# Kernel optimization log

Measured on AMD Instinct MI355X. Metric: run time of the kernel, lower is better.

## Reference

```python
import jax, jax.numpy as jnp
import numpy as np

BATCH = 4096
IN_SIZES = [1024, 1024, 1024, 1024]
EMB = 2048  # embracement_size


def setup_inputs() -> dict:
    key = jax.random.key(0)
    keys = jax.random.split(key, 3 * len(IN_SIZES))
    inp = {}
    for i, d in enumerate(IN_SIZES):
        inp[f"x{i}"] = jax.random.normal(keys[3 * i], (BATCH, d), dtype=jnp.float32)
        # Linear params (Kaiming-ish scale)
        inp[f"W{i}"] = jax.random.normal(keys[3 * i + 1], (d, EMB), dtype=jnp.float32) / np.sqrt(d)
        inp[f"b{i}"] = jax.random.normal(keys[3 * i + 2], (EMB,), dtype=jnp.float32) * 0.01
    return inp


def _sample_indices(batch, num_feats, emb):
    # availabilities=None, selection_probabilities=None -> uniform p over modalities
    # multinomial(p, num_samples=emb, replacement=True) == categorical over log p
    logits = jnp.zeros((batch, num_feats), dtype=jnp.float32)  # uniform
    k = jax.random.key(42)
    # shape (emb, batch) broadcasts against logits batch shape (batch,)
    idx = jax.random.categorical(k, logits, axis=-1, shape=(emb, batch))
    return idx.T  # [batch, emb]


def reference(x0, W0, b0, x1, W1, b1, x2, W2, b2, x3, W3, b3):
    xs = [x0, x1, x2, x3]
    Ws = [W0, W1, W2, W3]
    bs = [b0, b1, b2, b3]
    # docking: Linear + ReLU per modality -> [batch, EMB, num_feats]
    dock = jnp.stack([jax.nn.relu(x @ W + b) for x, W, b in zip(xs, Ws, bs)], axis=-1)
    B, E, F = dock.shape
    idx = _sample_indices(B, F, E)  # [B, E] int32
    # gather along modality axis (replaces one-hot multiply-sum)
    out = jnp.take_along_axis(dock, idx[:, :, None], axis=-1)[..., 0]
    return out  # [batch, EMB]
```

## Files before the change

### kernel.cpp

```cpp
#include <hip/hip_runtime.h>
#include <stdint.h>


typedef short short8 __attribute__((ext_vector_type(8)));
typedef float floatx4 __attribute__((ext_vector_type(4)));

#define B_DIM 4096
#define K_DIM 1024
#define E_DIM 2048

__device__ __forceinline__ uint16_t f2bf(float x) {
  uint32_t u = __float_as_uint(x);
  u += 0x7FFFu + ((u >> 16) & 1u);
  return (uint16_t)(u >> 16);
}

__device__ __forceinline__ void threefry(uint32_t x0, uint32_t x1,
                                         uint32_t& o0, uint32_t& o1) {
  const uint32_t ks0 = 0u;
  const uint32_t ks1 = 42u;
  const uint32_t ks2 = 0x1BD11BDAu ^ 42u;
  x0 += ks0; x1 += ks1;
#define TF_R(r) { x0 += x1; x1 = (x1 << r) | (x1 >> (32 - r)); x1 ^= x0; }
  TF_R(13) TF_R(15) TF_R(26) TF_R(6)
  x0 += ks1; x1 += ks2 + 1u;
  TF_R(17) TF_R(29) TF_R(16) TF_R(24)
  x0 += ks2; x1 += ks0 + 2u;
  TF_R(13) TF_R(15) TF_R(26) TF_R(6)
  x0 += ks0; x1 += ks1 + 3u;
  TF_R(17) TF_R(29) TF_R(16) TF_R(24)
  x0 += ks1; x1 += ks2 + 4u;
  TF_R(13) TF_R(15) TF_R(26) TF_R(6)
  x0 += ks2; x1 += ks0 + 5u;
#undef TF_R
  o0 = x0; o1 = x1;
}

__global__ __launch_bounds__(256) void prep_kernel(
    const float* __restrict__ x0, const float* __restrict__ x1,
    const float* __restrict__ x2, const float* __restrict__ x3,
    const float* __restrict__ W0, const float* __restrict__ W1,
    const float* __restrict__ W2, const float* __restrict__ W3,
    uint16_t* __restrict__ xb, uint16_t* __restrict__ Wt,
    uint32_t* __restrict__ idx2) {
  __shared__ float tile[32][33];
  const uint32_t g = blockIdx.x;
  const uint32_t chunk = g / 13u, slot = g % 13u;
  const int t = threadIdx.x;

  if (slot == 0) {
    uint32_t tid = chunk * 256u + t;
    uint32_t base = tid << 6;
    uint32_t word = 0;
#pragma unroll 4
    for (int j = 0; j < 16; ++j) {
      uint32_t c = base + 4u * j;
      uint32_t best = 0, bi = 0;
#pragma unroll
      for (uint32_t f = 0; f < 4; ++f) {
        uint32_t y0, y1;
        threefry(0u, c + f, y0, y1);
        uint32_t m = (y0 ^ y1) >> 9;
        if (f == 0) best = m;
        else if (m > best) { best = m; bi = f; }
      }
      word |= bi << (2 * j);
    }
    idx2[tid] = word;
  } else if (slot <= 8) {
    uint32_t xi = chunk * 8u + (slot - 1);
    int f = xi >> 12;
    const float* x = (f == 0) ? x0 : (f == 1) ? x1 : (f == 2) ? x2 : x3;
    size_t i = ((size_t)(xi & 4095) * 256 + t) * 4;
    float4 v = *(const float4*)(x + i);
    union { uint16_t h[4]; uint64_t q; } p;
    p.h[0] = f2bf(v.x); p.h[1] = f2bf(v.y);
    p.h[2] = f2bf(v.z); p.h[3] = f2bf(v.w);
    *(uint64_t*)(xb + (size_t)f * B_DIM * K_DIM + i) = p.q;
  } else {
    uint32_t wi = chunk * 4u + (slot - 9);
    int f = wi >> 11;
    uint32_t ip = wi & 2047;
    const float* W = (f == 0) ? W0 : (f == 1) ? W1 : (f == 2) ? W2 : W3;
    int e0 = (ip & 63) * 32, k0 = (ip >> 6) * 32;
    int tx = t & 31, ty = t >> 5;
#pragma unroll
    for (int i = 0; i < 4; ++i)
      tile[ty + i * 8][tx] = W[(size_t)(k0 + ty + i * 8) * E_DIM + e0 + tx];
    __syncthreads();
    int el = t >> 3, kc = (t & 7) * 4;
    union { uint16_t h[4]; uint64_t q; } p;
#pragma unroll
    for (int i = 0; i < 4; ++i) p.h[i] = f2bf(tile[kc + i][el]);
    uint16_t* dst = Wt + (size_t)f * E_DIM * K_DIM;
    *(uint64_t*)(dst + (size_t)(e0 + el) * K_DIM + k0 + kc) = p.q;
  }
}

__device__ __forceinline__ void async16(const uint16_t* g, uint16_t* lds) {
  __builtin_amdgcn_global_load_lds(
      (const __attribute__((address_space(1))) void*)g,
      (__attribute__((address_space(3))) void*)lds, 16, 0, 0);
}

__global__ __launch_bounds__(512, 4) void gemm_fused(
    const uint16_t* __restrict__ Ab, const uint16_t* __restrict__ Bbt,
    const uint32_t* __restrict__ idx2,
    const float* __restrict__ bias0, const float* __restrict__ bias1,
    const float* __restrict__ bias2, const float* __restrict__ bias3,
    float* __restrict__ out) {
  __shared__ uint16_t As[2][128 * 32];
  __shared__ uint16_t Bs[2][128 * 32];

  const int tid = threadIdx.x;
  const int w = tid >> 6;
  const int l = tid & 63;
  const int mBase = blockIdx.y * 128;
  const int nBase = blockIdx.x * 128;

  const int wm = (w >> 2) * 64;
  const int wn = (w & 3) * 32;
  const int sr = l >> 2;
  const int sc8 = (l & 3) ^ ((l >> 3) & 3);
  const int fr = l & 15, fq = l >> 4;
  const int fqs = (fq ^ ((fr >> 1) & 3)) * 8;

  const int b_hi0 = (mBase + wm) >> 4;
  uint32_t iw[2][4];
#pragma unroll
  for (int ni = 0; ni < 2; ++ni) {
    int col = nBase + wn + ni * 16 + fr;
#pragma unroll
    for (int mi = 0; mi < 4; ++mi)
      iw[ni][mi] = idx2[(size_t)col * (B_DIM / 16) + b_hi0 + mi];
  }

  floatx4 res[4][2] = {};

#pragma unroll 1
  for (int f = 0; f < 4; ++f) {
    const uint16_t* A = Ab  + (size_t)f * B_DIM * K_DIM + (size_t)mBase * K_DIM;
    const uint16_t* B = Bbt + (size_t)f * E_DIM * K_DIM + (size_t)nBase * K_DIM;
    const uint16_t* Aw = A + (size_t)(16 * w + sr) * K_DIM + sc8 * 8;
    const uint16_t* Bw = B + (size_t)(16 * w + sr) * K_DIM + sc8 * 8;

    floatx4 acc[4][2] = {};

    async16(Aw, &As[0][w * 512]);
    async16(Bw, &Bs[0][w * 512]);
    __syncthreads();

    int buf = 0;
#pragma unroll 1
    for (int kt = 0; kt < 32; ++kt) {
      int k0 = kt * 32;
      if (kt + 1 < 32) {
        async16(Aw + k0 + 32, &As[buf ^ 1][w * 512]);
        async16(Bw + k0 + 32, &Bs[buf ^ 1][w * 512]);
      }
      short8 a[4], b[2];
      #pragma unroll
      for (int mi = 0; mi < 4; ++mi)
        a[mi] = *(const short8*)&As[buf][(wm + mi * 16 + fr) * 32 + fqs];
      #pragma unroll
      for (int ni = 0; ni < 2; ++ni)
        b[ni] = *(const short8*)&Bs[buf][(wn + ni * 16 + fr) * 32 + fqs];
      #pragma unroll
      for (int mi = 0; mi < 4; ++mi)
        #pragma unroll
        for (int ni = 0; ni < 2; ++ni)
          acc[mi][ni] = __builtin_amdgcn_mfma_f32_16x16x32_bf16(
              a[mi], b[ni], acc[mi][ni], 0, 0, 0);
      __syncthreads();
      buf ^= 1;
    }

    const float* bias = (f == 0) ? bias0 : (f == 1) ? bias1
                      : (f == 2) ? bias2 : bias3;
    #pragma unroll
    for (int ni = 0; ni < 2; ++ni) {
      float bvf = bias[nBase + wn + ni * 16 + fr];
      #pragma unroll
      for (int mi = 0; mi < 4; ++mi) {
        uint32_t wd = iw[ni][mi];
        #pragma unroll
        for (int r = 0; r < 4; ++r) {
          uint32_t sel = (wd >> (2 * (fq * 4 + r))) & 3u;
          if (sel == (uint32_t)f) res[mi][ni][r] = acc[mi][ni][r] + bvf;
        }
      }
    }
  }

#pragma unroll
  for (int ni = 0; ni < 2; ++ni) {
    int col = nBase + wn + ni * 16 + fr;
#pragma unroll
    for (int mi = 0; mi < 4; ++mi) {
      int row0 = mBase + wm + mi * 16 + fq * 4;
#pragma unroll
      for (int r = 0; r < 4; ++r) {
        float o = res[mi][ni][r];
        __builtin_nontemporal_store(o > 0.f ? o : 0.f,
                                    &out[(size_t)(row0 + r) * E_DIM + col]);
      }
    }
  }
}

extern "C" void kernel_launch(void* const* d_in, const int* in_sizes, int n_in,
                              void* d_out, int out_size, void* d_ws, size_t ws_size,
                              hipStream_t stream) {
  const float* x[4]; const float* W[4]; const float* bs[4];
  for (int f = 0; f < 4; ++f) {
    x[f]  = (const float*)d_in[3 * f + 0];
    W[f]  = (const float*)d_in[3 * f + 1];
    bs[f] = (const float*)d_in[3 * f + 2];
  }
  char* ws = (char*)d_ws;
  uint16_t* xb  = (uint16_t*)ws;
  uint16_t* Wt  = (uint16_t*)(ws + (size_t)32 * 1024 * 1024);
  uint32_t* idx2 = (uint32_t*)(ws + (size_t)48 * 1024 * 1024);
  float* out = (float*)d_out;

  prep_kernel<<<dim3(26624), dim3(256), 0, stream>>>(
      x[0], x[1], x[2], x[3], W[0], W[1], W[2], W[3], xb, Wt, idx2);
  gemm_fused<<<dim3(E_DIM / 128, B_DIM / 128), dim3(512), 0, stream>>>(
      xb, Wt, idx2, bs[0], bs[1], bs[2], bs[3], out);
}
```

Before: 303.2 us.

## Use 4 waves with 64x64 warp tiles, drop LDS swizzle, use rotate builtin

```diff
diff --git a/kernel.cpp b/kernel.cpp
--- a/kernel.cpp
+++ b/kernel.cpp
@@ -8,6 +8,12 @@
 #define B_DIM 4096
 #define K_DIM 1024
 #define E_DIM 2048
+
+#if __has_builtin(__builtin_rotateleft32)
+#define ROTL32(x, r) __builtin_rotateleft32((x), (r))
+#else
+#define ROTL32(x, r) __builtin_amdgcn_alignbit((x), (x), 32 - (r))
+#endif
 
 __device__ __forceinline__ uint16_t f2bf(float x) {
   uint32_t u = __float_as_uint(x);
@@ -21,7 +27,7 @@
   const uint32_t ks1 = 42u;
   const uint32_t ks2 = 0x1BD11BDAu ^ 42u;
   x0 += ks0; x1 += ks1;
-#define TF_R(r) { x0 += x1; x1 = (x1 << r) | (x1 >> (32 - r)); x1 ^= x0; }
+#define TF_R(r) { x0 += x1; x1 = ROTL32(x1, r); x1 ^= x0; }
   TF_R(13) TF_R(15) TF_R(26) TF_R(6)
   x0 += ks1; x1 += ks2 + 1u;
   TF_R(17) TF_R(29) TF_R(16) TF_R(24)
@@ -103,7 +109,7 @@
       (__attribute__((address_space(3))) void*)lds, 16, 0, 0);
 }
 
-__global__ __launch_bounds__(512, 4) void gemm_fused(
+__global__ __launch_bounds__(256, 2) void gemm_fused(
     const uint16_t* __restrict__ Ab, const uint16_t* __restrict__ Bbt,
     const uint32_t* __restrict__ idx2,
     const float* __restrict__ bias0, const float* __restrict__ bias1,
@@ -118,57 +124,61 @@
   const int mBase = blockIdx.y * 128;
   const int nBase = blockIdx.x * 128;
 
-  const int wm = (w >> 2) * 64;
-  const int wn = (w & 3) * 32;
-  const int sr = l >> 2;
-  const int sc8 = (l & 3) ^ ((l >> 3) & 3);
+  const int wm = (w >> 1) * 64, wn = (w & 1) * 64;
+  const int sr = l >> 2, sc8 = l & 3;
   const int fr = l & 15, fq = l >> 4;
-  const int fqs = (fq ^ ((fr >> 1) & 3)) * 8;
+  const int c0 = 2 * w, c1 = 2 * w + 1;
 
   const int b_hi0 = (mBase + wm) >> 4;
-  uint32_t iw[2][4];
-#pragma unroll
-  for (int ni = 0; ni < 2; ++ni) {
+  uint32_t iw[4][4];
+#pragma unroll
+  for (int ni = 0; ni < 4; ++ni) {
     int col = nBase + wn + ni * 16 + fr;
 #pragma unroll
     for (int mi = 0; mi < 4; ++mi)
       iw[ni][mi] = idx2[(size_t)col * (B_DIM / 16) + b_hi0 + mi];
   }
 
-  floatx4 res[4][2] = {};
+  floatx4 res[4][4] = {};
 
 #pragma unroll 1
   for (int f = 0; f < 4; ++f) {
     const uint16_t* A = Ab  + (size_t)f * B_DIM * K_DIM + (size_t)mBase * K_DIM;
     const uint16_t* B = Bbt + (size_t)f * E_DIM * K_DIM + (size_t)nBase * K_DIM;
-    const uint16_t* Aw = A + (size_t)(16 * w + sr) * K_DIM + sc8 * 8;
-    const uint16_t* Bw = B + (size_t)(16 * w + sr) * K_DIM + sc8 * 8;
-
-    floatx4 acc[4][2] = {};
-
-    async16(Aw, &As[0][w * 512]);
-    async16(Bw, &Bs[0][w * 512]);
+    const uint16_t* Ap0 = A + (size_t)(c0 * 16 + sr) * K_DIM + sc8 * 8;
+    const uint16_t* Ap1 = A + (size_t)(c1 * 16 + sr) * K_DIM + sc8 * 8;
+    const uint16_t* Bp0 = B + (size_t)(c0 * 16 + sr) * K_DIM + sc8 * 8;
+    const uint16_t* Bp1 = B + (size_t)(c1 * 16 + sr) * K_DIM + sc8 * 8;
+
+    floatx4 acc[4][4] = {};
+
+    async16(Ap0, &As[0][c0 * 512]);
+    async16(Ap1, &As[0][c1 * 512]);
+    async16(Bp0, &Bs[0][c0 * 512]);
+    async16(Bp1, &Bs[0][c1 * 512]);
     __syncthreads();
 
     int buf = 0;
 #pragma unroll 1
     for (int kt = 0; kt < 32; ++kt) {
-      int k0 = kt * 32;
+      int kn = (kt + 1) * 32;
       if (kt + 1 < 32) {
-        async16(Aw + k0 + 32, &As[buf ^ 1][w * 512]);
-        async16(Bw + k0 + 32, &Bs[buf ^ 1][w * 512]);
-      }
-      short8 a[4], b[2];
+        async16(Ap0 + kn, &As[buf ^ 1][c0 * 512]);
+        async16(Ap1 + kn, &As[buf ^ 1][c1 * 512]);
+        async16(Bp0 + kn, &Bs[buf ^ 1][c0 * 512]);
+        async16(Bp1 + kn, &Bs[buf ^ 1][c1 * 512]);
+      }
+      short8 a[4], b[4];
       #pragma unroll
       for (int mi = 0; mi < 4; ++mi)
-        a[mi] = *(const short8*)&As[buf][(wm + mi * 16 + fr) * 32 + fqs];
-      #pragma unroll
-      for (int ni = 0; ni < 2; ++ni)
-        b[ni] = *(const short8*)&Bs[buf][(wn + ni * 16 + fr) * 32 + fqs];
+        a[mi] = *(const short8*)&As[buf][(wm + mi * 16 + fr) * 32 + fq * 8];
+      #pragma unroll
+      for (int ni = 0; ni < 4; ++ni)
+        b[ni] = *(const short8*)&Bs[buf][(wn + ni * 16 + fr) * 32 + fq * 8];
       #pragma unroll
       for (int mi = 0; mi < 4; ++mi)
         #pragma unroll
-        for (int ni = 0; ni < 2; ++ni)
+        for (int ni = 0; ni < 4; ++ni)
           acc[mi][ni] = __builtin_amdgcn_mfma_f32_16x16x32_bf16(
               a[mi], b[ni], acc[mi][ni], 0, 0, 0);
       __syncthreads();
@@ -178,7 +188,7 @@
     const float* bias = (f == 0) ? bias0 : (f == 1) ? bias1
                       : (f == 2) ? bias2 : bias3;
     #pragma unroll
-    for (int ni = 0; ni < 2; ++ni) {
+    for (int ni = 0; ni < 4; ++ni) {
       float bvf = bias[nBase + wn + ni * 16 + fr];
       #pragma unroll
       for (int mi = 0; mi < 4; ++mi) {
@@ -193,7 +203,7 @@
   }
 
 #pragma unroll
-  for (int ni = 0; ni < 2; ++ni) {
+  for (int ni = 0; ni < 4; ++ni) {
     int col = nBase + wn + ni * 16 + fr;
 #pragma unroll
     for (int mi = 0; mi < 4; ++mi) {
@@ -225,6 +235,6 @@
 
   prep_kernel<<<dim3(26624), dim3(256), 0, stream>>>(
       x[0], x[1], x[2], x[3], W[0], W[1], W[2], W[3], xb, Wt, idx2);
-  gemm_fused<<<dim3(E_DIM / 128, B_DIM / 128), dim3(512), 0, stream>>>(
+  gemm_fused<<<dim3(E_DIM / 128, B_DIM / 128), dim3(256), 0, stream>>>(
       xb, Wt, idx2, bs[0], bs[1], bs[2], bs[3], out);
 }
```

Result: slower. 309.4 us (+2.0%).
